# Kernel optimization log

Hardware: AMD Instinct MI355X
Metric: run time of the kernel (lower is better)

The kernel has to match this reference:

```python
import jax, jax.numpy as jnp
import numpy as np


def setup_inputs() -> dict:
    key = jax.random.key(0)
    ks = jax.random.split(key, 6)
    B, H, F, X, T = 8, 32, 8, 128, 256
    z0 = jax.random.normal(ks[0], (B, H, X), jnp.float32)
    xi = jax.random.normal(ks[1], (B, F, X, T), jnp.float32)
    A = jax.random.normal(ks[2], (H, H), jnp.float32) * 0.1
    Gw = jax.random.normal(ks[3], (H, F, H), jnp.float32) * 0.1
    Wr = jax.random.normal(ks[4], (X, H, H, H), jnp.float32) * 1e-4
    Wi = jax.random.normal(ks[5], (X, H, H, H), jnp.float32) * 1e-4
    return {"z0": z0, "xi": xi, "A": A, "Gw": Gw, "Wr": Wr, "Wi": Wi}


def reference(z0, xi, A, Gw, Wr, Wi):
    # z0: (B, H, X); xi: (B, F, X, T)
    B, Hc, X = z0.shape
    T = xi.shape[-1]

    # Initial guess u(t) = z0 for all t (reconstruction of the fixed-point seed).
    u = jnp.broadcast_to(z0[..., None], (B, Hc, X, T))

    # Linear SPDE right-hand side: Fu = A u, Gu = Gw u.
    Fu = jnp.einsum('ih,bhxt->bixt', A, u)
    Gu = jnp.einsum('ifh,bhxt->bifxt', Gw, u)          # (B, H, F, X, T)
    Guxi = jnpum = None
    Guxi = jnp.einsum('bifxt,bfxt->bixt', Gu, xi)
    Hu = Fu + Guxi                                      # (B, H, X, T)

    # Spatial FFT (axis 2) + fftshift, as in the torch module.
    H_ft = jnp.fft.fftshift(jnp.fft.fft(Hu, axis=2), axes=2)    # complex64
    z0_ft = jnp.fft.fftshift(jnp.fft.fft(z0, axis=2), axes=2)   # (B, H, X)

    # Per-Fourier-mode complex-linear CDE vector field weights.
    W = (Wr + 1j * Wi).astype(jnp.complex64)            # (X, H, H, H)

    # Control path X(t): (B, X, T, H); Euler increments at the knots.
    Hp = jnp.transpose(H_ft, (0, 2, 3, 1))
    dX = Hp[:, :, 1:, :] - Hp[:, :, :-1, :]             # (B, X, T-1, H)
    z_init = jnp.transpose(z0_ft, (0, 2, 1))            # (B, X, H)

    def step(z, dx):
        # f(z)[b, x, i, c] = sum_j W[x, i, c, j] z[b, x, j]
        fz = jnp.einsum('xicj,bxj->bxic', W, z)
        z_new = z + jnp.einsum('bxic,bxc->bxi', fz, dx)  # dz = f(z) . dX
        return z_new, z_new

    _, zs = jax.lax.scan(step, z_init, jnp.moveaxis(dX, 2, 0))
    zs = jnp.concatenate([z_init[None], zs], axis=0)    # (T, B, X, H)
    z_all = jnp.transpose(zs, (1, 3, 2, 0))             # (B, H, X, T)

    u_new = jnp.fft.ifft(jnp.fft.ifftshift(z_all, axes=2), axis=2)
    return u_new.real
```

## Files before the change

kernel.cpp:

```cpp
#include <hip/hip_runtime.h>
#include <math.h>

#define Bc 8
#define Hc 32
#define Fc 8
#define Xc 128
#define Tc 256

typedef __bf16 bf16x8 __attribute__((ext_vector_type(8)));
typedef float f32x4 __attribute__((ext_vector_type(4)));

__device__ __forceinline__ int bitrev7(int x) { return (int)(__brev((unsigned)x) >> 25); }

__device__ __forceinline__ unsigned pack_bf16(float a, float b) {
    unsigned ua = __float_as_uint(a);
    unsigned ub = __float_as_uint(b);
    ua = (ua + 0x7FFFu + ((ua >> 16) & 1u)) >> 16;
    ub = (ub + 0x7FFFu + ((ub >> 16) & 1u)) & 0xFFFF0000u;
    return (ua & 0xFFFFu) | ub;
}
__device__ __forceinline__ float bf16_val(float a) {
    unsigned ua = __float_as_uint(a);
    ua = (ua + 0x7FFFu + ((ua >> 16) & 1u)) & 0xFFFF0000u;
    return __uint_as_float(ua);
}

__device__ __forceinline__ void bfly(float2& a, float2& b, float2 twv, float sign) {
    float cs = twv.x, sn = sign * twv.y;
    float2 bw = make_float2(cs * b.x - sn * b.y, cs * b.y + sn * b.x);
    float2 na = make_float2(a.x + bw.x, a.y + bw.y);
    b = make_float2(a.x - bw.x, a.y - bw.y);
    a = na;
}

template <int NTHR>
__device__ __forceinline__ void fft32x128(float2* buf, float sign) {
    __shared__ float2 tw[128];
    int tid = threadIdx.x;
    if (tid >= 1 && tid < 128) {
        int h = 1 << (31 - __builtin_clz((unsigned)tid));
        int pos = tid - h;
        float sn, cs;
        __sincosf(3.14159265358979f * (float)pos / (float)h, &sn, &cs);
        tw[tid] = make_float2(cs, sn);
    }
    __syncthreads();
    for (int grp = tid; grp < 32 * 16; grp += NTHR) {
        float2* p = buf + grp * 8;
        float2 v[8];
#pragma unroll
        for (int e = 0; e < 8; ++e) v[e] = p[e];
        bfly(v[0], v[1], tw[1], sign); bfly(v[2], v[3], tw[1], sign);
        bfly(v[4], v[5], tw[1], sign); bfly(v[6], v[7], tw[1], sign);
        bfly(v[0], v[2], tw[2], sign); bfly(v[1], v[3], tw[3], sign);
        bfly(v[4], v[6], tw[2], sign); bfly(v[5], v[7], tw[3], sign);
        bfly(v[0], v[4], tw[4], sign); bfly(v[1], v[5], tw[5], sign);
        bfly(v[2], v[6], tw[6], sign); bfly(v[3], v[7], tw[7], sign);
#pragma unroll
        for (int e = 0; e < 8; ++e) p[e] = v[e];
    }
    __syncthreads();
    for (int grp = tid; grp < 32 * 32; grp += NTHR) {
        int row = grp >> 5, sub = grp & 31;
        int m = sub & 7, k = sub >> 3;
        float2* p = buf + row * 128 + k * 32 + m;
        float2 v0 = p[0], v1 = p[8], v2 = p[16], v3 = p[24];
        bfly(v0, v1, tw[8 + m], sign);
        bfly(v2, v3, tw[8 + m], sign);
        bfly(v0, v2, tw[16 + m], sign);
        bfly(v1, v3, tw[16 + m + 8], sign);
        p[0] = v0; p[8] = v1; p[16] = v2; p[24] = v3;
    }
    __syncthreads();
    for (int grp = tid; grp < 32 * 32; grp += NTHR) {
        int row = grp >> 5, m2 = grp & 31;
        float2* p = buf + row * 128 + m2;
        float2 v0 = p[0], v1 = p[32], v2 = p[64], v3 = p[96];
        bfly(v0, v1, tw[32 + m2], sign);
        bfly(v2, v3, tw[32 + m2], sign);
        bfly(v0, v2, tw[64 + m2], sign);
        bfly(v1, v3, tw[64 + m2 + 32], sign);
        p[0] = v0; p[32] = v1; p[64] = v2; p[96] = v3;
    }
    __syncthreads();
}

__global__ void k_xit(const float* __restrict__ xi, float* __restrict__ xiT) {
    __shared__ float tile[32][33];
    int bid = blockIdx.x;
    int bf = bid >> 3, tt = bid & 7;
    int t0 = tt * 32;
    int tid = threadIdx.x;
    for (int xt = 0; xt < 4; ++xt) {
        int x0 = xt * 32;
        __syncthreads();
        for (int idx = tid; idx < 1024; idx += 256) {
            int xr = idx >> 5, tc = idx & 31;
            tile[xr][tc] = xi[((size_t)bf * Xc + x0 + xr) * Tc + t0 + tc];
        }
        __syncthreads();
        for (int idx = tid; idx < 1024; idx += 256) {
            int tr = idx >> 5, xc = idx & 31;
            xiT[((size_t)bf * Tc + t0 + tr) * Xc + x0 + xc] = tile[xc][tr];
        }
    }
}

__global__ void k_pre(const float* __restrict__ z0, const float* __restrict__ A,
                      const float* __restrict__ Gw, float* __restrict__ Fz,
                      float* __restrict__ Gz, float2* __restrict__ Z0ft) {
    __shared__ float z0l[Hc * Xc];
    __shared__ float2 cbuf[Hc * Xc];
    int b = blockIdx.x;
    int tid = threadIdx.x;
    for (int idx = tid; idx < Hc * Xc; idx += 256) z0l[idx] = z0[b * Hc * Xc + idx];
    __syncthreads();
    for (int idx = tid; idx < Hc * Xc; idx += 256) {
        int i = idx >> 7, x = idx & 127;
        float s = 0.f;
        for (int h = 0; h < Hc; ++h) s += A[i * Hc + h] * z0l[h * 128 + x];
        Fz[b * Hc * Xc + idx] = s;
    }
    for (int idx = tid; idx < Hc * Fc * Xc; idx += 256) {
        int i = idx >> 10, f = (idx >> 7) & 7, x = idx & 127;
        float s = 0.f;
        for (int h = 0; h < Hc; ++h) s += Gw[(i * Fc + f) * Hc + h] * z0l[h * 128 + x];
        Gz[b * Hc * Fc * Xc + idx] = s;
    }
    for (int idx = tid; idx < Hc * Xc; idx += 256) {
        int h = idx >> 7, x = idx & 127;
        cbuf[h * 128 + bitrev7(x)] = make_float2(z0l[h * 128 + x], 0.f);
    }
    fft32x128<256>(cbuf, -1.f);
    for (int idx = tid; idx < Xc * Hc; idx += 256) {
        int xs = idx >> 5, h = idx & 31;
        Z0ft[(b * Xc + xs) * Hc + h] = cbuf[h * 128 + ((xs + 64) & 127)];
    }
}

__global__ void k_spec(const float* __restrict__ xiT, const float* __restrict__ Fz,
                       const float* __restrict__ Gz, float2* __restrict__ Hft) {
    __shared__ float xil[Fc * Xc];
    __shared__ float2 cbuf[Hc * Xc];
    int bid = blockIdx.x;
    int b = bid >> 8, t = bid & 255;
    int tid = threadIdx.x;
    for (int idx = tid; idx < Fc * Xc; idx += 512) {
        int f = idx >> 7, x = idx & 127;
        xil[idx] = xiT[((size_t)(b * Fc + f) * Tc + t) * Xc + x];
    }
    __syncthreads();
    for (int idx = tid; idx < Hc * Xc; idx += 512) {
        int i = idx >> 7, x = idx & 127;
        float hu = Fz[b * Hc * Xc + idx];
        const float* gzp = Gz + (b * Hc + i) * (Fc * Xc) + x;
#pragma unroll
        for (int f = 0; f < Fc; ++f) hu += gzp[f * 128] * xil[f * 128 + x];
        cbuf[i * 128 + bitrev7(x)] = make_float2(hu, 0.f);
    }
    fft32x128<512>(cbuf, -1.f);
    for (int idx = tid; idx < Xc * Hc; idx += 512) {
        int xs = idx >> 5, i = idx & 31;
        Hft[((long)(b * Xc + xs) * Tc + t) * Hc + i] = cbuf[i * 128 + ((xs + 64) & 127)];
    }
}

#define ML_DW 16448
#define B_DW  1152
#define SCAN_LDS 150016

__device__ __forceinline__ void build_B(unsigned* Bb, int w, int tt, int c,
                                        float2 hp, float2 hn, float sc) {
    float dre = (hn.x - hp.x) * sc;
    float dim = (hn.y - hp.y) * sc;
    float hre = bf16_val(dre), hmim = bf16_val(-dim), him = bf16_val(dim);
    int n0 = w * 4 + tt * 2;
    Bb[n0 * 36 + c] = pack_bf16(hre, hmim);
    Bb[(n0 + 1) * 36 + c] = pack_bf16(him, hre);
    Bb[576 + n0 * 36 + c] = pack_bf16(dre - hre, (-dim) - hmim);
    Bb[576 + (n0 + 1) * 36 + c] = pack_bf16(dim - him, dre - hre);
}

__global__ __launch_bounds__(768, 3) void k_scan(const float* __restrict__ Wr,
                                                 const float* __restrict__ Wi,
                                                 const float2* __restrict__ Hft,
                                                 const float2* __restrict__ Z0ft,
                                                 float2* __restrict__ Zall) {
    extern __shared__ unsigned char smem[];
    float* Mlf = (float*)smem;
    unsigned* Aw = (unsigned*)smem;
    unsigned* Bd = (unsigned*)(smem + 131584);
    float* zlf = (float*)(smem + 140800);
    float2* zstc = (float2*)(smem + 141824);

    int tid = threadIdx.x;
    int x = blockIdx.x >> 1, g = blockIdx.x & 1;
    int lane = tid & 63, wid = tid >> 6;
    int isProd = (wid < 8);
    int p = wid;
    int w = isProd ? (wid & 3) : (wid - 8);
    int b = g * 4 + w;

    const float* wrp = Wr + (size_t)x * 32768;
    const float* wip = Wi + (size_t)x * 32768;
    for (int idx = tid; idx < 32768; idx += 768) {
        int j = idx & 31, cc = (idx >> 5) & 31, ii = idx >> 10;
        int r = ii * 32 + j;
        int pd = r * 32 + (((cc >> 2) ^ (r & 7)) << 2) + (cc & 3);
        Aw[pd] = pack_bf16(wrp[(ii * 32 + cc) * 32 + j], wip[(ii * 32 + cc) * 32 + j]);
    }
    __syncthreads();

    size_t bx = (size_t)(b * Xc + x);
    const float2* Hrow = Hft + bx * (Tc * Hc);
    float2* Zrow = Zall + bx * (Hc * Tc);
    int jq = lane >> 5, il = lane & 31;

    uint4 af[8][2];
    float2 Hp2 = make_float2(0.f, 0.f), Hn2 = make_float2(0.f, 0.f);
    float2 zr = make_float2(0.f, 0.f);

    if (isProd) {
        int n16 = lane & 15, q = lane >> 4;
        int rbase = p * 128 + n16;
#pragma unroll
        for (int mt = 0; mt < 8; ++mt) {
            int r = rbase + mt * 16;
#pragma unroll
            for (int kf = 0; kf < 2; ++kf) {
                int cg = (kf * 4 + q) ^ (r & 7);
                af[mt][kf] = *(const uint4*)(Aw + r * 32 + cg * 4);
            }
        }
    } else {
        zr = Z0ft[bx * Hc + il];
        if (jq == 0) {
            ((float2*)(zlf + w * 64))[il] = zr;
            zstc[w * 256 + il] = zr;
        }
        float2 ha = Hrow[jq * 32 + il];
        float2 hb = Hrow[(1 + jq) * 32 + il];
        build_B(Bd, w, jq, il, ha, hb, 1.f);
        Hp2 = Hrow[(2 + jq) * 32 + il];
        Hn2 = Hrow[(3 + jq) * 32 + il];
    }
    __syncthreads();

#pragma unroll 1
    for (int k = 0; k <= 128; ++k) {
        if (isProd) {
            if (k < 128) {
                int bk = k & 1;
                int n = lane & 15, q = lane >> 4;
                const unsigned* Bb = Bd + bk * B_DW;
                bf16x8 bh0 = __builtin_bit_cast(bf16x8, *(const uint4*)(Bb + n * 36 + q * 4));
                bf16x8 bh1 = __builtin_bit_cast(bf16x8, *(const uint4*)(Bb + n * 36 + 16 + q * 4));
                bf16x8 bl0 = __builtin_bit_cast(bf16x8, *(const uint4*)(Bb + 576 + n * 36 + q * 4));
                bf16x8 bl1 = __builtin_bit_cast(bf16x8, *(const uint4*)(Bb + 576 + n * 36 + 16 + q * 4));
                float* Mb = Mlf + bk * ML_DW;
#pragma unroll
                for (int mt = 0; mt < 8; ++mt) {
                    f32x4 acc = {0.f, 0.f, 0.f, 0.f};
                    acc = __builtin_amdgcn_mfma_f32_16x16x32_bf16(
                        __builtin_bit_cast(bf16x8, af[mt][0]), bh0, acc, 0, 0, 0);
                    acc = __builtin_amdgcn_mfma_f32_16x16x32_bf16(
                        __builtin_bit_cast(bf16x8, af[mt][1]), bh1, acc, 0, 0, 0);
                    acc = __builtin_amdgcn_mfma_f32_16x16x32_bf16(
                        __builtin_bit_cast(bf16x8, af[mt][0]), bl0, acc, 0, 0, 0);
                    acc = __builtin_amdgcn_mfma_f32_16x16x32_bf16(
                        __builtin_bit_cast(bf16x8, af[mt][1]), bl1, acc, 0, 0, 0);
                    int i = p * 4 + (mt >> 1);
                    int jgp = (((mt & 1) * 4) + q) ^ (i & 7);
                    *(f32x4*)(Mb + n * 1028 + i * 32 + jgp * 4) = acc;
                }
            }
        } else {
            float2 HpN = Hp2, HnN = Hn2;
            if (k + 2 <= 127) {
                int kc2 = k + 2;
                HpN = Hrow[(2 * kc2 + jq) * 32 + il];
                int t2 = 2 * kc2 + 1 + jq;
                if (t2 > 255) t2 = 255;
                HnN = Hrow[t2 * 32 + il];
            }
            if (k > 0) {
                int kc = k - 1;
                int bk = kc & 1;
#pragma unroll
                for (int s = 0; s < 2; ++s) {
                    int t = 2 * kc + 1 + s;
                    if (t > 255) break;
                    const float* base = Mlf + bk * ML_DW + (w * 4 + s * 2) * 1028 + il * 32;
                    float4 mr[4], mi[4];
#pragma unroll
                    for (int gg = 0; gg < 4; ++gg) {
                        int jg = (((jq * 4 + gg) ^ (il & 7)) << 2);
                        mr[gg] = *(const float4*)(base + jg);
                        mi[gg] = *(const float4*)(base + 1028 + jg);
                    }
                    const float4* zf4 = (const float4*)(zlf + w * 64);
                    float yR = 0.f, yI = 0.f;
#pragma unroll
                    for (int gg = 0; gg < 4; ++gg) {
                        float4 za = zf4[jq * 8 + gg * 2];
                        float4 zb = zf4[jq * 8 + gg * 2 + 1];
                        yR += mr[gg].x * za.x - mi[gg].x * za.y + mr[gg].y * za.z - mi[gg].y * za.w
                            + mr[gg].z * zb.x - mi[gg].z * zb.y + mr[gg].w * zb.z - mi[gg].w * zb.w;
                        yI += mr[gg].x * za.y + mi[gg].x * za.x + mr[gg].y * za.w + mi[gg].y * za.z
                            + mr[gg].z * zb.y + mi[gg].z * zb.x + mr[gg].w * zb.w + mi[gg].w * zb.z;
                    }
                    yR += __shfl_xor(yR, 32);
                    yI += __shfl_xor(yI, 32);
                    zr.x += yR;
                    zr.y += yI;
                    if (jq == 0) {
                        ((float2*)(zlf + w * 64))[il] = zr;
                        zstc[w * 256 + (t & 7) * 32 + il] = zr;
                    }
                    if ((t & 7) == 7) {
                        int t0 = t - 7;
                        int i2 = lane >> 1, tb = (lane & 1) * 4;
                        float2 v0 = zstc[w * 256 + (tb + 0) * 32 + i2];
                        float2 v1 = zstc[w * 256 + (tb + 1) * 32 + i2];
                        float2 v2 = zstc[w * 256 + (tb + 2) * 32 + i2];
                        float2 v3 = zstc[w * 256 + (tb + 3) * 32 + i2];
                        *(float4*)(Zrow + i2 * Tc + t0 + tb) = make_float4(v0.x, v0.y, v1.x, v1.y);
                        *(float4*)(Zrow + i2 * Tc + t0 + tb + 2) = make_float4(v2.x, v2.y, v3.x, v3.y);
                    }
                }
            }
            if (k < 127) {
                float sc = (2 * (k + 1) + 1 + jq <= 255) ? 1.f : 0.f;
                build_B(Bd + ((k + 1) & 1) * B_DW, w, jq, il, Hp2, Hn2, sc);
                Hp2 = HpN;
                Hn2 = HnN;
            }
        }
        __syncthreads();
    }
}

__global__ void k_post(const float2* __restrict__ Zall, float* __restrict__ out) {
    __shared__ float2 cbuf[32 * 128];
    int bid = blockIdx.x;
    int b = bid >> 8, i = (bid >> 3) & 31, tq = bid & 7;
    int t0 = tq * 32;
    int tid = threadIdx.x;
    for (int idx = tid; idx < 128 * 32; idx += 512) {
        int k = idx >> 5, tc = idx & 31;
        int xg = (k + 64) & 127;
        cbuf[tc * 128 + bitrev7(k)] =
            Zall[((long)(b * Xc + xg) * Hc + i) * Tc + t0 + tc];
    }
    fft32x128<512>(cbuf, +1.f);
    const float inv = 1.0f / 128.0f;
    for (int idx = tid; idx < 128 * 32; idx += 512) {
        int xs = idx >> 5, tc = idx & 31;
        out[((long)(b * Hc + i) * Xc + xs) * Tc + t0 + tc] = cbuf[tc * 128 + xs].x * inv;
    }
}

extern "C" void kernel_launch(void* const* d_in, const int* in_sizes, int n_in,
                              void* d_out, int out_size, void* d_ws, size_t ws_size,
                              hipStream_t stream) {
    const float* z0 = (const float*)d_in[0];
    const float* xi = (const float*)d_in[1];
    const float* A = (const float*)d_in[2];
    const float* Gw = (const float*)d_in[3];
    const float* Wr = (const float*)d_in[4];
    const float* Wi = (const float*)d_in[5];
    float* out = (float*)d_out;
    char* ws = (char*)d_ws;

    float2* Hft = (float2*)(ws);
    float2* Zall = (float2*)(ws + 67108864);
    float2* Z0ft = (float2*)(ws + 134217728);
    float* Fz = (float*)(ws + 134479872);
    float* Gz = (float*)(ws + 134610944);
    float* xiT = (float*)(ws + 67108864);

    (void)hipFuncSetAttribute((const void*)k_scan,
                              hipFuncAttributeMaxDynamicSharedMemorySize, SCAN_LDS);

    k_xit<<<Bc * Fc * 8, 256, 0, stream>>>(xi, xiT);
    k_pre<<<Bc, 256, 0, stream>>>(z0, A, Gw, Fz, Gz, Z0ft);
    k_spec<<<Bc * Tc, 512, 0, stream>>>(xiT, Fz, Gz, Hft);
    k_scan<<<Xc * 2, 768, SCAN_LDS, stream>>>(Wr, Wi, Hft, Z0ft, Zall);
    k_post<<<Bc * Hc * 8, 512, 0, stream>>>(Zall, out);
}
```

Before: 455.5 us.

## Pad FFT shared rows, vectorize spec/post loads, extra swizzle, raise scan priority

Pads the shared FFT buffer rows to 129 complex elements so that column-wise accesses in the FFT and in the transposed read-outs hit different LDS banks. Vectorizes the xi/Fz/Gz loads in k_spec and the Zall loads in k_post to float4. Adds a second XOR term to the swizzle of the M tile written by the producer and read by the consumer in the scan, and raises wave priority for the consumer waves. Together these target LDS bank conflicts and load instruction count, at the cost of slightly more shared memory and more index arithmetic.

```diff
diff --git a/kernel.cpp b/kernel.cpp
--- a/kernel.cpp
+++ b/kernel.cpp
@@ -33,6 +33,7 @@
     a = na;
 }
 
+#define FRS 129
 template <int NTHR>
 __device__ __forceinline__ void fft32x128(float2* buf, float sign) {
     __shared__ float2 tw[128];
@@ -46,7 +47,7 @@
     }
     __syncthreads();
     for (int grp = tid; grp < 32 * 16; grp += NTHR) {
-        float2* p = buf + grp * 8;
+        float2* p = buf + (grp >> 4) * FRS + (grp & 15) * 8;
         float2 v[8];
 #pragma unroll
         for (int e = 0; e < 8; ++e) v[e] = p[e];
@@ -63,7 +64,7 @@
     for (int grp = tid; grp < 32 * 32; grp += NTHR) {
         int row = grp >> 5, sub = grp & 31;
         int m = sub & 7, k = sub >> 3;
-        float2* p = buf + row * 128 + k * 32 + m;
+        float2* p = buf + row * FRS + k * 32 + m;
         float2 v0 = p[0], v1 = p[8], v2 = p[16], v3 = p[24];
         bfly(v0, v1, tw[8 + m], sign);
         bfly(v2, v3, tw[8 + m], sign);
@@ -74,7 +75,7 @@
     __syncthreads();
     for (int grp = tid; grp < 32 * 32; grp += NTHR) {
         int row = grp >> 5, m2 = grp & 31;
-        float2* p = buf + row * 128 + m2;
+        float2* p = buf + row * FRS + m2;
         float2 v0 = p[0], v1 = p[32], v2 = p[64], v3 = p[96];
         bfly(v0, v1, tw[32 + m2], sign);
         bfly(v2, v3, tw[32 + m2], sign);
@@ -110,7 +111,7 @@
                       const float* __restrict__ Gw, float* __restrict__ Fz,
                       float* __restrict__ Gz, float2* __restrict__ Z0ft) {
     __shared__ float z0l[Hc * Xc];
-    __shared__ float2 cbuf[Hc * Xc];
+    __shared__ float2 cbuf[Hc * FRS];
     int b = blockIdx.x;
     int tid = threadIdx.x;
     for (int idx = tid; idx < Hc * Xc; idx += 256) z0l[idx] = z0[b * Hc * Xc + idx];
@@ -129,39 +130,48 @@
     }
     for (int idx = tid; idx < Hc * Xc; idx += 256) {
         int h = idx >> 7, x = idx & 127;
-        cbuf[h * 128 + bitrev7(x)] = make_float2(z0l[h * 128 + x], 0.f);
+        cbuf[h * FRS + bitrev7(x)] = make_float2(z0l[h * 128 + x], 0.f);
     }
     fft32x128<256>(cbuf, -1.f);
     for (int idx = tid; idx < Xc * Hc; idx += 256) {
         int xs = idx >> 5, h = idx & 31;
-        Z0ft[(b * Xc + xs) * Hc + h] = cbuf[h * 128 + ((xs + 64) & 127)];
+        Z0ft[(b * Xc + xs) * Hc + h] = cbuf[h * FRS + ((xs + 64) & 127)];
     }
 }
 
 __global__ void k_spec(const float* __restrict__ xiT, const float* __restrict__ Fz,
                        const float* __restrict__ Gz, float2* __restrict__ Hft) {
     __shared__ float xil[Fc * Xc];
-    __shared__ float2 cbuf[Hc * Xc];
+    __shared__ float2 cbuf[Hc * FRS];
     int bid = blockIdx.x;
     int b = bid >> 8, t = bid & 255;
     int tid = threadIdx.x;
-    for (int idx = tid; idx < Fc * Xc; idx += 512) {
-        int f = idx >> 7, x = idx & 127;
-        xil[idx] = xiT[((size_t)(b * Fc + f) * Tc + t) * Xc + x];
-    }
-    __syncthreads();
-    for (int idx = tid; idx < Hc * Xc; idx += 512) {
-        int i = idx >> 7, x = idx & 127;
-        float hu = Fz[b * Hc * Xc + idx];
-        const float* gzp = Gz + (b * Hc + i) * (Fc * Xc) + x;
-#pragma unroll
-        for (int f = 0; f < Fc; ++f) hu += gzp[f * 128] * xil[f * 128 + x];
-        cbuf[i * 128 + bitrev7(x)] = make_float2(hu, 0.f);
+    for (int idx = tid; idx < Fc * Xc / 4; idx += 512) {
+        int f = idx >> 5, xq = (idx & 31) * 4;
+        *(float4*)(xil + f * 128 + xq) =
+            *(const float4*)(xiT + ((size_t)(b * Fc + f) * Tc + t) * Xc + xq);
+    }
+    __syncthreads();
+    for (int idx = tid; idx < Hc * Xc / 4; idx += 512) {
+        int i = idx >> 5, xq = (idx & 31) * 4;
+        float4 hu = *(const float4*)(Fz + b * Hc * Xc + i * 128 + xq);
+        const float* gzp = Gz + (b * Hc + i) * (Fc * Xc) + xq;
+#pragma unroll
+        for (int f = 0; f < Fc; ++f) {
+            float4 gz = *(const float4*)(gzp + f * 128);
+            float4 xv = *(const float4*)(&xil[f * 128 + xq]);
+            hu.x += gz.x * xv.x; hu.y += gz.y * xv.y;
+            hu.z += gz.z * xv.z; hu.w += gz.w * xv.w;
+        }
+        cbuf[i * FRS + bitrev7(xq + 0)] = make_float2(hu.x, 0.f);
+        cbuf[i * FRS + bitrev7(xq + 1)] = make_float2(hu.y, 0.f);
+        cbuf[i * FRS + bitrev7(xq + 2)] = make_float2(hu.z, 0.f);
+        cbuf[i * FRS + bitrev7(xq + 3)] = make_float2(hu.w, 0.f);
     }
     fft32x128<512>(cbuf, -1.f);
     for (int idx = tid; idx < Xc * Hc; idx += 512) {
         int xs = idx >> 5, i = idx & 31;
-        Hft[((long)(b * Xc + xs) * Tc + t) * Hc + i] = cbuf[i * 128 + ((xs + 64) & 127)];
+        Hft[((long)(b * Xc + xs) * Tc + t) * Hc + i] = cbuf[i * FRS + ((xs + 64) & 127)];
     }
 }
 
@@ -233,6 +243,7 @@
             }
         }
     } else {
+        __builtin_amdgcn_s_setprio(1);
         zr = Z0ft[bx * Hc + il];
         if (jq == 0) {
             ((float2*)(zlf + w * 64))[il] = zr;
@@ -270,7 +281,7 @@
                     acc = __builtin_amdgcn_mfma_f32_16x16x32_bf16(
                         __builtin_bit_cast(bf16x8, af[mt][1]), bl1, acc, 0, 0, 0);
                     int i = p * 4 + (mt >> 1);
-                    int jgp = (((mt & 1) * 4) + q) ^ (i & 7);
+                    int jgp = ((((mt & 1) * 4) + q) ^ (i & 7)) ^ ((i >> 3) & 3);
                     *(f32x4*)(Mb + n * 1028 + i * 32 + jgp * 4) = acc;
                 }
             }
@@ -294,7 +305,7 @@
                     float4 mr[4], mi[4];
 #pragma unroll
                     for (int gg = 0; gg < 4; ++gg) {
-                        int jg = (((jq * 4 + gg) ^ (il & 7)) << 2);
+                        int jg = (((jq * 4 + gg) ^ (il & 7) ^ ((il >> 3) & 3)) << 2);
                         mr[gg] = *(const float4*)(base + jg);
                         mi[gg] = *(const float4*)(base + 1028 + jg);
                     }
@@ -341,22 +352,24 @@
 }
 
 __global__ void k_post(const float2* __restrict__ Zall, float* __restrict__ out) {
-    __shared__ float2 cbuf[32 * 128];
+    __shared__ float2 cbuf[32 * FRS];
     int bid = blockIdx.x;
     int b = bid >> 8, i = (bid >> 3) & 31, tq = bid & 7;
     int t0 = tq * 32;
     int tid = threadIdx.x;
-    for (int idx = tid; idx < 128 * 32; idx += 512) {
-        int k = idx >> 5, tc = idx & 31;
+    for (int idx = tid; idx < 128 * 16; idx += 512) {
+        int k = idx >> 4, tc2 = (idx & 15) * 2;
         int xg = (k + 64) & 127;
-        cbuf[tc * 128 + bitrev7(k)] =
-            Zall[((long)(b * Xc + xg) * Hc + i) * Tc + t0 + tc];
+        float4 v = *(const float4*)(Zall + ((long)(b * Xc + xg) * Hc + i) * Tc + t0 + tc2);
+        int kb = bitrev7(k);
+        cbuf[tc2 * FRS + kb] = make_float2(v.x, v.y);
+        cbuf[(tc2 + 1) * FRS + kb] = make_float2(v.z, v.w);
     }
     fft32x128<512>(cbuf, +1.f);
     const float inv = 1.0f / 128.0f;
     for (int idx = tid; idx < 128 * 32; idx += 512) {
         int xs = idx >> 5, tc = idx & 31;
-        out[((long)(b * Hc + i) * Xc + xs) * Tc + t0 + tc] = cbuf[tc * 128 + xs].x * inv;
+        out[((long)(b * Hc + i) * Xc + xs) * Tc + t0 + tc] = cbuf[tc * FRS + xs].x * inv;
     }
 }
 
```

New measurement: 414.2 us (median of 2 runs). 9.1% less time.
